# Performance work log

Hardware: AMD Instinct MI355X
Metric: run time of the kernel (lower is better)

## Reference

```python
import jax, jax.numpy as jnp
import numpy as np

HUGE_FLOAT = 1000.0
B, LATENT, N, EMB, NBOND = 256, 256, 64, 64, 5


def setup_inputs() -> dict:
    key = jax.random.key(0)
    ks = jax.random.split(key, 8)
    s1 = 1.0 / np.sqrt(LATENT)
    s2 = 1.0 / np.sqrt(2 * EMB)
    s3 = 1.0 / np.sqrt(EMB)
    return {
        "z": jax.random.normal(ks[0], (B, LATENT), dtype=jnp.float32),
        "num_real_atoms": jax.random.randint(ks[1], (B,), 1, N + 1, dtype=jnp.int32),
        "W_nodes": jax.random.uniform(ks[2], (LATENT, N * EMB), jnp.float32, -s1, s1),
        "b_nodes": jax.random.uniform(ks[3], (N * EMB,), jnp.float32, -s1, s1),
        "W1": jax.random.uniform(ks[4], (2 * EMB, EMB), jnp.float32, -s2, s2),
        "b1": jax.random.uniform(ks[5], (EMB,), jnp.float32, -s2, s2),
        "W2": jax.random.uniform(ks[6], (EMB, NBOND), jnp.float32, -s3, s3),
        "b2": jax.random.uniform(ks[7], (NBOND,), jnp.float32, -s3, s3),
    }


def reference(z, num_real_atoms, W_nodes, b_nodes, W1, b1, W2, b2):
    # z: (B, latent) -> node embeddings h: (B, N, emb)
    h = (z @ W_nodes + b_nodes).reshape(B, N, EMB)
    # edge MLP first layer on concat([h_i, h_j]) == h_i @ W1a + h_j @ W1b
    W1a, W1b = W1[:EMB], W1[EMB:]
    a = jnp.einsum("bne,ef->bnf", h, W1a)  # (B, N, emb)
    c = jnp.einsum("bne,ef->bnf", h, W1b)  # (B, N, emb)
    hidden = jax.nn.relu(a[:, :, None, :] + c[:, None, :, :] + b1)  # (B,N,N,emb)
    logits = jnp.einsum("bijf,fk->bijk", hidden, W2) + b2  # (B,N,N,5)
    # diagonal mask + padding mask (symmetric), constant fill per bond channel
    diag = jnp.eye(N, dtype=bool)  # (N,N)
    real = jnp.arange(N)[None, :] < num_real_atoms[:, None]  # (B,N)
    pad = ~real
    padding = pad[:, :, None] | pad[:, None, :]  # (B,N,N)
    mask = diag[None] | padding  # (B,N,N)
    fill = jnp.where(jnp.arange(NBOND) == NBOND - 1, HUGE_FLOAT, -HUGE_FLOAT).astype(logits.dtype)
    logits = jnp.where(mask[..., None], fill, logits)
    # symmetrize over node pair dims
    return 0.5 * (logits + jnp.swapaxes(logits, 1, 2))
```

## Files before the change

kernel.cpp:

```cpp
#include <hip/hip_runtime.h>
#include <hip/hip_bf16.h>

#define HUGEF 1000.0f

typedef __hip_bfloat16 bf16;

__device__ __forceinline__ float b2f(bf16 x) { return __bfloat162float(x); }

__global__ __launch_bounds__(256) void k_hac(
    const float* __restrict__ z, const float* __restrict__ Wn,
    const float* __restrict__ bn, const float* __restrict__ W1,
    const float* __restrict__ b1, bf16* __restrict__ a_ws,
    bf16* __restrict__ c_ws)
{
    __shared__ float buf0[64][68];
    __shared__ float buf1[64][68];
    __shared__ float buf2[64][68];

    const int t = threadIdx.x;
    const int tx = t & 15, ty = t >> 4;
    const int atom = blockIdx.x;
    const int m0 = blockIdx.y * 64;
    const int n0 = atom * 64;

    float acc[4][4] = {};
    for (int k0 = 0; k0 < 256; k0 += 64) {
        __syncthreads();
        #pragma unroll
        for (int r = 0; r < 4; ++r) {
            int q = t + 256 * r;
            int m = q >> 4, kk = (q & 15) * 4;
            *(float4*)&buf0[m][kk] = *(const float4*)&z[(m0 + m) * 256 + k0 + kk];
        }
        #pragma unroll
        for (int r = 0; r < 4; ++r) {
            int q = t + 256 * r;
            int k = q >> 4, nn = (q & 15) * 4;
            *(float4*)&buf1[k][nn] = *(const float4*)&Wn[(k0 + k) * 4096 + n0 + nn];
        }
        __syncthreads();
        for (int k = 0; k < 64; ++k) {
            float4 bv = *(const float4*)&buf1[k][tx * 4];
            float bb[4] = {bv.x, bv.y, bv.z, bv.w};
            float aa[4];
            #pragma unroll
            for (int i = 0; i < 4; ++i) aa[i] = buf0[ty * 4 + i][k];
            #pragma unroll
            for (int i = 0; i < 4; ++i)
                #pragma unroll
                for (int jj = 0; jj < 4; ++jj) acc[i][jj] += aa[i] * bb[jj];
        }
    }
    __syncthreads();

    {
        float bnv[4];
        #pragma unroll
        for (int jj = 0; jj < 4; ++jj) bnv[jj] = bn[n0 + tx * 4 + jj];
        #pragma unroll
        for (int i = 0; i < 4; ++i)
            #pragma unroll
            for (int jj = 0; jj < 4; ++jj)
                buf2[ty * 4 + i][tx * 4 + jj] = acc[i][jj] + bnv[jj];
        #pragma unroll
        for (int r = 0; r < 4; ++r) {
            int q = t + 256 * r;
            int e = q >> 4, ff = (q & 15) * 4;
            *(float4*)&buf0[e][ff] = *(const float4*)&W1[4 * q];
            *(float4*)&buf1[e][ff] = *(const float4*)&W1[4096 + 4 * q];
        }
    }
    __syncthreads();

    float aacc[4][4] = {}, cacc[4][4] = {};
    const int b0 = ty * 4, f0 = tx * 4;
    for (int e = 0; e < 64; ++e) {
        float4 wa = *(const float4*)&buf0[e][f0];
        float4 wb = *(const float4*)&buf1[e][f0];
        float wav[4] = {wa.x, wa.y, wa.z, wa.w};
        float wbv[4] = {wb.x, wb.y, wb.z, wb.w};
        #pragma unroll
        for (int i = 0; i < 4; ++i) {
            float hv = buf2[b0 + i][e];
            #pragma unroll
            for (int jj = 0; jj < 4; ++jj) {
                aacc[i][jj] += hv * wav[jj];
                cacc[i][jj] += hv * wbv[jj];
            }
        }
    }
    float b1v[4];
    #pragma unroll
    for (int jj = 0; jj < 4; ++jj) b1v[jj] = b1[f0 + jj];
    #pragma unroll
    for (int i = 0; i < 4; ++i) {
        int bi = m0 + b0 + i;
        int idx = bi * 4096 + n0 + f0;
        ushort4 av, cv;
        av.x = __bfloat16_as_ushort(__float2bfloat16(aacc[i][0] + b1v[0]));
        av.y = __bfloat16_as_ushort(__float2bfloat16(aacc[i][1] + b1v[1]));
        av.z = __bfloat16_as_ushort(__float2bfloat16(aacc[i][2] + b1v[2]));
        av.w = __bfloat16_as_ushort(__float2bfloat16(aacc[i][3] + b1v[3]));
        cv.x = __bfloat16_as_ushort(__float2bfloat16(cacc[i][0]));
        cv.y = __bfloat16_as_ushort(__float2bfloat16(cacc[i][1]));
        cv.z = __bfloat16_as_ushort(__float2bfloat16(cacc[i][2]));
        cv.w = __bfloat16_as_ushort(__float2bfloat16(cacc[i][3]));
        *(ushort4*)&a_ws[idx] = av;
        *(ushort4*)&c_ws[idx] = cv;
    }
}

__global__ __launch_bounds__(256) void k_pairs(
    const bf16* __restrict__ a_ws, const bf16* __restrict__ c_ws,
    const int* __restrict__ nra, const float* __restrict__ W2,
    const float* __restrict__ b2, float* __restrict__ out)
{
    __shared__ float as[64][68];
    __shared__ float cs[64][68];
    __shared__ float w2t[5][68];

    const int t = threadIdx.x;
    const int bid = blockIdx.x;
    const int b = bid >> 2;
    const int ic = bid & 3;
    const int n = nra[b];

    #pragma unroll
    for (int r = 0; r < 4; ++r) {
        int q = t + 256 * r;
        int atom = q >> 4, ff = (q & 15) * 4;
        ushort4 av = *(const ushort4*)&a_ws[b * 4096 + 4 * q];
        ushort4 cv = *(const ushort4*)&c_ws[b * 4096 + 4 * q];
        as[atom][ff + 0] = b2f(__ushort_as_bfloat16(av.x));
        as[atom][ff + 1] = b2f(__ushort_as_bfloat16(av.y));
        as[atom][ff + 2] = b2f(__ushort_as_bfloat16(av.z));
        as[atom][ff + 3] = b2f(__ushort_as_bfloat16(av.w));
        cs[atom][ff + 0] = b2f(__ushort_as_bfloat16(cv.x));
        cs[atom][ff + 1] = b2f(__ushort_as_bfloat16(cv.y));
        cs[atom][ff + 2] = b2f(__ushort_as_bfloat16(cv.z));
        cs[atom][ff + 3] = b2f(__ushort_as_bfloat16(cv.w));
    }
    if (t < 64) {
        #pragma unroll
        for (int k = 0; k < 5; ++k) w2t[k][t] = W2[t * 5 + k];
    }
    float b2v[5];
    #pragma unroll
    for (int k = 0; k < 5; ++k) b2v[k] = b2[k];
    __syncthreads();

    const int j = t & 63;
    const int wq = t >> 6;
    const float fillv[5] = {-HUGEF, -HUGEF, -HUGEF, -HUGEF, HUGEF};

    #pragma unroll 1
    for (int q = 0; q < 4; ++q) {
        const int i = ic * 16 + wq * 4 + q;
        float* op = out + ((b * 64 + i) * 64 + j) * 5;
        if (i >= n) {
            #pragma unroll
            for (int k = 0; k < 5; ++k) op[k] = fillv[k];
            continue;
        }
        float acc[5] = {0.f, 0.f, 0.f, 0.f, 0.f};
        for (int f4 = 0; f4 < 64; f4 += 4) {
            float4 ai = *(const float4*)&as[i][f4];
            float4 ci = *(const float4*)&cs[i][f4];
            float4 aj = *(const float4*)&as[j][f4];
            float4 cj = *(const float4*)&cs[j][f4];
            float s0 = fmaxf(ai.x + cj.x, 0.f) + fmaxf(aj.x + ci.x, 0.f);
            float s1 = fmaxf(ai.y + cj.y, 0.f) + fmaxf(aj.y + ci.y, 0.f);
            float s2 = fmaxf(ai.z + cj.z, 0.f) + fmaxf(aj.z + ci.z, 0.f);
            float s3 = fmaxf(ai.w + cj.w, 0.f) + fmaxf(aj.w + ci.w, 0.f);
            #pragma unroll
            for (int k = 0; k < 5; ++k) {
                float4 w = *(const float4*)&w2t[k][f4];
                acc[k] += s0 * w.x + s1 * w.y + s2 * w.z + s3 * w.w;
            }
        }
        const bool masked = (j == i) || (j >= n);
        #pragma unroll
        for (int k = 0; k < 5; ++k) {
            float v = masked ? fillv[k] : (0.5f * acc[k] + b2v[k]);
            op[k] = v;
        }
    }
}

extern "C" void kernel_launch(void* const* d_in, const int* in_sizes, int n_in,
                              void* d_out, int out_size, void* d_ws, size_t ws_size,
                              hipStream_t stream)
{
    const float* z  = (const float*)d_in[0];
    const int*   nra = (const int*)d_in[1];
    const float* Wn = (const float*)d_in[2];
    const float* bn = (const float*)d_in[3];
    const float* W1 = (const float*)d_in[4];
    const float* b1 = (const float*)d_in[5];
    const float* W2 = (const float*)d_in[6];
    const float* b2 = (const float*)d_in[7];
    float* out = (float*)d_out;

    bf16* a_ws = (bf16*)d_ws;
    bf16* c_ws = a_ws + 256 * 4096;

    hipLaunchKernelGGL(k_hac, dim3(64, 4), dim3(256), 0, stream,
                       z, Wn, bn, W1, b1, a_ws, c_ws);
    hipLaunchKernelGGL(k_pairs, dim3(1024), dim3(256), 0, stream,
                       a_ws, c_ws, nra, W2, b2, out);
}
```

Baseline: 118.4 us.

## Use bf16 MFMA for node/edge GMMs and register-block pair kernel

The first kernel now converts z, W_nodes and W1 to bf16 in shared memory and computes both matmuls with 16x16x32 bf16 MFMA instructions instead of scalar FMA loops. This reduces scalar compute but lowers the precision of the node embeddings. The pair kernel keeps a/c as packed bf16 in shared memory, unpacking with shifts. Each thread now computes 8 rows i, reusing j-side values and W2 loads across them, with half as many blocks and early exit for fully padded row groups.

```diff
diff --git a/kernel.cpp b/kernel.cpp
--- a/kernel.cpp
+++ b/kernel.cpp
@@ -4,8 +4,18 @@
 #define HUGEF 1000.0f
 
 typedef __hip_bfloat16 bf16;
-
-__device__ __forceinline__ float b2f(bf16 x) { return __bfloat162float(x); }
+typedef __attribute__((ext_vector_type(8))) short short8;
+typedef __attribute__((ext_vector_type(4))) float floatx4;
+
+__device__ __forceinline__ ushort f2bf(float x) {
+    return __bfloat16_as_ushort(__float2bfloat16(x));
+}
+__device__ __forceinline__ float bflo(unsigned u) {
+    return __uint_as_float(u << 16);
+}
+__device__ __forceinline__ float bfhi(unsigned u) {
+    return __uint_as_float(u & 0xffff0000u);
+}
 
 __global__ __launch_bounds__(256) void k_hac(
     const float* __restrict__ z, const float* __restrict__ Wn,
@@ -13,100 +23,107 @@
     const float* __restrict__ b1, bf16* __restrict__ a_ws,
     bf16* __restrict__ c_ws)
 {
-    __shared__ float buf0[64][68];
-    __shared__ float buf1[64][68];
-    __shared__ float buf2[64][68];
+    __shared__ ushort zt[64][136];
+    __shared__ ushort wnt[64][136];
+    __shared__ ushort ht[64][72];
+    __shared__ ushort w1at[64][72];
+    __shared__ ushort w1bt[64][72];
 
     const int t = threadIdx.x;
-    const int tx = t & 15, ty = t >> 4;
+    const int lane = t & 63;
+    const int wv = t >> 6;
+    const int l15 = lane & 15;
+    const int quad = lane >> 4;
     const int atom = blockIdx.x;
     const int m0 = blockIdx.y * 64;
     const int n0 = atom * 64;
 
-    float acc[4][4] = {};
-    for (int k0 = 0; k0 < 256; k0 += 64) {
+    {
+        const int f = t & 63;
+        const int g = t >> 6;
+        #pragma unroll
+        for (int qq = 0; qq < 4; ++qq) {
+            int e = g * 16 + qq * 4;
+            ushort4 va, vb;
+            va.x = f2bf(W1[(e + 0) * 64 + f]);
+            va.y = f2bf(W1[(e + 1) * 64 + f]);
+            va.z = f2bf(W1[(e + 2) * 64 + f]);
+            va.w = f2bf(W1[(e + 3) * 64 + f]);
+            vb.x = f2bf(W1[(64 + e + 0) * 64 + f]);
+            vb.y = f2bf(W1[(64 + e + 1) * 64 + f]);
+            vb.z = f2bf(W1[(64 + e + 2) * 64 + f]);
+            vb.w = f2bf(W1[(64 + e + 3) * 64 + f]);
+            *(ushort4*)&w1at[f][e] = va;
+            *(ushort4*)&w1bt[f][e] = vb;
+        }
+    }
+
+    floatx4 acc1[4] = {};
+    for (int kt = 0; kt < 256; kt += 128) {
         __syncthreads();
         #pragma unroll
+        for (int r = 0; r < 8; ++r) {
+            int q = t + 256 * r;
+            int m = q >> 5, kk = (q & 31) * 4;
+            float4 v = *(const float4*)&z[(m0 + m) * 256 + kt + kk];
+            ushort4 u = {f2bf(v.x), f2bf(v.y), f2bf(v.z), f2bf(v.w)};
+            *(ushort4*)&zt[m][kk] = u;
+        }
+        {
+            int n = t & 63, g = t >> 6;
+            #pragma unroll
+            for (int qq = 0; qq < 8; ++qq) {
+                int k = g * 32 + qq * 4;
+                const float* p = &Wn[(size_t)(kt + k) * 4096 + n0 + n];
+                ushort4 u = {f2bf(p[0]), f2bf(p[4096]),
+                             f2bf(p[2 * 4096]), f2bf(p[3 * 4096])};
+                *(ushort4*)&wnt[n][k] = u;
+            }
+        }
+        __syncthreads();
+        #pragma unroll
+        for (int ks = 0; ks < 4; ++ks) {
+            short8 a = *(const short8*)&zt[wv * 16 + l15][ks * 32 + quad * 8];
+            #pragma unroll
+            for (int nt = 0; nt < 4; ++nt) {
+                short8 bf = *(const short8*)&wnt[nt * 16 + l15][ks * 32 + quad * 8];
+                acc1[nt] = __builtin_amdgcn_mfma_f32_16x16x32_bf16(a, bf, acc1[nt], 0, 0, 0);
+            }
+        }
+    }
+
+    #pragma unroll
+    for (int nt = 0; nt < 4; ++nt) {
+        float bnv = bn[n0 + nt * 16 + l15];
+        #pragma unroll
+        for (int r = 0; r < 4; ++r)
+            ht[wv * 16 + quad * 4 + r][nt * 16 + l15] = f2bf(acc1[nt][r] + bnv);
+    }
+    __syncthreads();
+
+    floatx4 acc2a[4] = {}, acc2c[4] = {};
+    #pragma unroll
+    for (int ks = 0; ks < 2; ++ks) {
+        short8 a = *(const short8*)&ht[wv * 16 + l15][ks * 32 + quad * 8];
+        #pragma unroll
+        for (int ft = 0; ft < 4; ++ft) {
+            short8 ba = *(const short8*)&w1at[ft * 16 + l15][ks * 32 + quad * 8];
+            short8 bb = *(const short8*)&w1bt[ft * 16 + l15][ks * 32 + quad * 8];
+            acc2a[ft] = __builtin_amdgcn_mfma_f32_16x16x32_bf16(a, ba, acc2a[ft], 0, 0, 0);
+            acc2c[ft] = __builtin_amdgcn_mfma_f32_16x16x32_bf16(a, bb, acc2c[ft], 0, 0, 0);
+        }
+    }
+
+    #pragma unroll
+    for (int ft = 0; ft < 4; ++ft) {
+        float b1v = b1[ft * 16 + l15];
+        #pragma unroll
         for (int r = 0; r < 4; ++r) {
-            int q = t + 256 * r;
-            int m = q >> 4, kk = (q & 15) * 4;
-            *(float4*)&buf0[m][kk] = *(const float4*)&z[(m0 + m) * 256 + k0 + kk];
-        }
-        #pragma unroll
-        for (int r = 0; r < 4; ++r) {
-            int q = t + 256 * r;
-            int k = q >> 4, nn = (q & 15) * 4;
-            *(float4*)&buf1[k][nn] = *(const float4*)&Wn[(k0 + k) * 4096 + n0 + nn];
-        }
-        __syncthreads();
-        for (int k = 0; k < 64; ++k) {
-            float4 bv = *(const float4*)&buf1[k][tx * 4];
-            float bb[4] = {bv.x, bv.y, bv.z, bv.w};
-            float aa[4];
-            #pragma unroll
-            for (int i = 0; i < 4; ++i) aa[i] = buf0[ty * 4 + i][k];
-            #pragma unroll
-            for (int i = 0; i < 4; ++i)
-                #pragma unroll
-                for (int jj = 0; jj < 4; ++jj) acc[i][jj] += aa[i] * bb[jj];
-        }
-    }
-    __syncthreads();
-
-    {
-        float bnv[4];
-        #pragma unroll
-        for (int jj = 0; jj < 4; ++jj) bnv[jj] = bn[n0 + tx * 4 + jj];
-        #pragma unroll
-        for (int i = 0; i < 4; ++i)
-            #pragma unroll
-            for (int jj = 0; jj < 4; ++jj)
-                buf2[ty * 4 + i][tx * 4 + jj] = acc[i][jj] + bnv[jj];
-        #pragma unroll
-        for (int r = 0; r < 4; ++r) {
-            int q = t + 256 * r;
-            int e = q >> 4, ff = (q & 15) * 4;
-            *(float4*)&buf0[e][ff] = *(const float4*)&W1[4 * q];
-            *(float4*)&buf1[e][ff] = *(const float4*)&W1[4096 + 4 * q];
-        }
-    }
-    __syncthreads();
-
-    float aacc[4][4] = {}, cacc[4][4] = {};
-    const int b0 = ty * 4, f0 = tx * 4;
-    for (int e = 0; e < 64; ++e) {
-        float4 wa = *(const float4*)&buf0[e][f0];
-        float4 wb = *(const float4*)&buf1[e][f0];
-        float wav[4] = {wa.x, wa.y, wa.z, wa.w};
-        float wbv[4] = {wb.x, wb.y, wb.z, wb.w};
-        #pragma unroll
-        for (int i = 0; i < 4; ++i) {
-            float hv = buf2[b0 + i][e];
-            #pragma unroll
-            for (int jj = 0; jj < 4; ++jj) {
-                aacc[i][jj] += hv * wav[jj];
-                cacc[i][jj] += hv * wbv[jj];
-            }
-        }
-    }
-    float b1v[4];
-    #pragma unroll
-    for (int jj = 0; jj < 4; ++jj) b1v[jj] = b1[f0 + jj];
-    #pragma unroll
-    for (int i = 0; i < 4; ++i) {
-        int bi = m0 + b0 + i;
-        int idx = bi * 4096 + n0 + f0;
-        ushort4 av, cv;
-        av.x = __bfloat16_as_ushort(__float2bfloat16(aacc[i][0] + b1v[0]));
-        av.y = __bfloat16_as_ushort(__float2bfloat16(aacc[i][1] + b1v[1]));
-        av.z = __bfloat16_as_ushort(__float2bfloat16(aacc[i][2] + b1v[2]));
-        av.w = __bfloat16_as_ushort(__float2bfloat16(aacc[i][3] + b1v[3]));
-        cv.x = __bfloat16_as_ushort(__float2bfloat16(cacc[i][0]));
-        cv.y = __bfloat16_as_ushort(__float2bfloat16(cacc[i][1]));
-        cv.z = __bfloat16_as_ushort(__float2bfloat16(cacc[i][2]));
-        cv.w = __bfloat16_as_ushort(__float2bfloat16(cacc[i][3]));
-        *(ushort4*)&a_ws[idx] = av;
-        *(ushort4*)&c_ws[idx] = cv;
+            int m = wv * 16 + quad * 4 + r;
+            size_t idx = (size_t)(m0 + m) * 4096 + n0 + ft * 16 + l15;
+            a_ws[idx] = __float2bfloat16(acc2a[ft][r] + b1v);
+            c_ws[idx] = __float2bfloat16(acc2c[ft][r]);
+        }
     }
 }
 
@@ -115,30 +132,23 @@
     const int* __restrict__ nra, const float* __restrict__ W2,
     const float* __restrict__ b2, float* __restrict__ out)
 {
-    __shared__ float as[64][68];
-    __shared__ float cs[64][68];
+    __shared__ unsigned ap[64][36];
+    __shared__ unsigned cp[64][36];
     __shared__ float w2t[5][68];
 
     const int t = threadIdx.x;
-    const int bid = blockIdx.x;
-    const int b = bid >> 2;
-    const int ic = bid & 3;
+    const int b = blockIdx.x >> 1;
+    const int ic = blockIdx.x & 1;
     const int n = nra[b];
 
-    #pragma unroll
-    for (int r = 0; r < 4; ++r) {
+    const ushort* ag = (const ushort*)a_ws + (size_t)b * 4096;
+    const ushort* cg = (const ushort*)c_ws + (size_t)b * 4096;
+    #pragma unroll
+    for (int r = 0; r < 2; ++r) {
         int q = t + 256 * r;
-        int atom = q >> 4, ff = (q & 15) * 4;
-        ushort4 av = *(const ushort4*)&a_ws[b * 4096 + 4 * q];
-        ushort4 cv = *(const ushort4*)&c_ws[b * 4096 + 4 * q];
-        as[atom][ff + 0] = b2f(__ushort_as_bfloat16(av.x));
-        as[atom][ff + 1] = b2f(__ushort_as_bfloat16(av.y));
-        as[atom][ff + 2] = b2f(__ushort_as_bfloat16(av.z));
-        as[atom][ff + 3] = b2f(__ushort_as_bfloat16(av.w));
-        cs[atom][ff + 0] = b2f(__ushort_as_bfloat16(cv.x));
-        cs[atom][ff + 1] = b2f(__ushort_as_bfloat16(cv.y));
-        cs[atom][ff + 2] = b2f(__ushort_as_bfloat16(cv.z));
-        cs[atom][ff + 3] = b2f(__ushort_as_bfloat16(cv.w));
+        int atom = q >> 3, wq = (q & 7) * 4;
+        *(uint4*)&ap[atom][wq] = *(const uint4*)&ag[atom * 64 + wq * 2];
+        *(uint4*)&cp[atom][wq] = *(const uint4*)&cg[atom * 64 + wq * 2];
     }
     if (t < 64) {
         #pragma unroll
@@ -150,39 +160,74 @@
     __syncthreads();
 
     const int j = t & 63;
-    const int wq = t >> 6;
+    const int wv = t >> 6;
+    const int i0 = ic * 32 + wv * 8;
     const float fillv[5] = {-HUGEF, -HUGEF, -HUGEF, -HUGEF, HUGEF};
 
-    #pragma unroll 1
-    for (int q = 0; q < 4; ++q) {
-        const int i = ic * 16 + wq * 4 + q;
-        float* op = out + ((b * 64 + i) * 64 + j) * 5;
+    if (i0 >= n) {
+        #pragma unroll
+        for (int r = 0; r < 8; ++r) {
+            float* op = out + ((size_t)(b * 64 + i0 + r) * 64 + j) * 5;
+            #pragma unroll
+            for (int k = 0; k < 5; ++k) op[k] = fillv[k];
+        }
+        return;
+    }
+
+    float acc[8][5] = {};
+    for (int w8 = 0; w8 < 8; ++w8) {
+        uint4 ajp = *(const uint4*)&ap[j][w8 * 4];
+        uint4 cjp = *(const uint4*)&cp[j][w8 * 4];
+        float ajv[8], cjv[8];
+        ajv[0] = bflo(ajp.x); ajv[1] = bfhi(ajp.x);
+        ajv[2] = bflo(ajp.y); ajv[3] = bfhi(ajp.y);
+        ajv[4] = bflo(ajp.z); ajv[5] = bfhi(ajp.z);
+        ajv[6] = bflo(ajp.w); ajv[7] = bfhi(ajp.w);
+        cjv[0] = bflo(cjp.x); cjv[1] = bfhi(cjp.x);
+        cjv[2] = bflo(cjp.y); cjv[3] = bfhi(cjp.y);
+        cjv[4] = bflo(cjp.z); cjv[5] = bfhi(cjp.z);
+        cjv[6] = bflo(cjp.w); cjv[7] = bfhi(cjp.w);
+        float4 wA[5], wB[5];
+        #pragma unroll
+        for (int k = 0; k < 5; ++k) {
+            wA[k] = *(const float4*)&w2t[k][w8 * 8];
+            wB[k] = *(const float4*)&w2t[k][w8 * 8 + 4];
+        }
+        #pragma unroll
+        for (int r = 0; r < 8; ++r) {
+            uint4 aip = *(const uint4*)&ap[i0 + r][w8 * 4];
+            uint4 cip = *(const uint4*)&cp[i0 + r][w8 * 4];
+            float s[8];
+            s[0] = fmaxf(bflo(aip.x) + cjv[0], 0.f) + fmaxf(ajv[0] + bflo(cip.x), 0.f);
+            s[1] = fmaxf(bfhi(aip.x) + cjv[1], 0.f) + fmaxf(ajv[1] + bfhi(cip.x), 0.f);
+            s[2] = fmaxf(bflo(aip.y) + cjv[2], 0.f) + fmaxf(ajv[2] + bflo(cip.y), 0.f);
+            s[3] = fmaxf(bfhi(aip.y) + cjv[3], 0.f) + fmaxf(ajv[3] + bfhi(cip.y), 0.f);
+            s[4] = fmaxf(bflo(aip.z) + cjv[4], 0.f) + fmaxf(ajv[4] + bflo(cip.z), 0.f);
+            s[5] = fmaxf(bfhi(aip.z) + cjv[5], 0.f) + fmaxf(ajv[5] + bfhi(cip.z), 0.f);
+            s[6] = fmaxf(bflo(aip.w) + cjv[6], 0.f) + fmaxf(ajv[6] + bflo(cip.w), 0.f);
+            s[7] = fmaxf(bfhi(aip.w) + cjv[7], 0.f) + fmaxf(ajv[7] + bfhi(cip.w), 0.f);
+            #pragma unroll
+            for (int k = 0; k < 5; ++k) {
+                acc[r][k] += s[0] * wA[k].x + s[1] * wA[k].y +
+                             s[2] * wA[k].z + s[3] * wA[k].w +
+                             s[4] * wB[k].x + s[5] * wB[k].y +
+                             s[6] * wB[k].z + s[7] * wB[k].w;
+            }
+        }
+    }
+
+    #pragma unroll
+    for (int r = 0; r < 8; ++r) {
+        const int i = i0 + r;
+        float* op = out + ((size_t)(b * 64 + i) * 64 + j) * 5;
         if (i >= n) {
             #pragma unroll
             for (int k = 0; k < 5; ++k) op[k] = fillv[k];
-            continue;
-        }
-        float acc[5] = {0.f, 0.f, 0.f, 0.f, 0.f};
-        for (int f4 = 0; f4 < 64; f4 += 4) {
-            float4 ai = *(const float4*)&as[i][f4];
-            float4 ci = *(const float4*)&cs[i][f4];
-            float4 aj = *(const float4*)&as[j][f4];
-            float4 cj = *(const float4*)&cs[j][f4];
-            float s0 = fmaxf(ai.x + cj.x, 0.f) + fmaxf(aj.x + ci.x, 0.f);
-            float s1 = fmaxf(ai.y + cj.y, 0.f) + fmaxf(aj.y + ci.y, 0.f);
-            float s2 = fmaxf(ai.z + cj.z, 0.f) + fmaxf(aj.z + ci.z, 0.f);
-            float s3 = fmaxf(ai.w + cj.w, 0.f) + fmaxf(aj.w + ci.w, 0.f);
-            #pragma unroll
-            for (int k = 0; k < 5; ++k) {
-                float4 w = *(const float4*)&w2t[k][f4];
-                acc[k] += s0 * w.x + s1 * w.y + s2 * w.z + s3 * w.w;
-            }
-        }
-        const bool masked = (j == i) || (j >= n);
-        #pragma unroll
-        for (int k = 0; k < 5; ++k) {
-            float v = masked ? fillv[k] : (0.5f * acc[k] + b2v[k]);
-            op[k] = v;
+        } else {
+            const bool masked = (j == i) || (j >= n);
+            #pragma unroll
+            for (int k = 0; k < 5; ++k)
+                op[k] = masked ? fillv[k] : (0.5f * acc[r][k] + b2v[k]);
         }
     }
 }
@@ -206,6 +251,6 @@
 
     hipLaunchKernelGGL(k_hac, dim3(64, 4), dim3(256), 0, stream,
                        z, Wn, bn, W1, b1, a_ws, c_ws);
-    hipLaunchKernelGGL(k_pairs, dim3(1024), dim3(256), 0, stream,
+    hipLaunchKernelGGL(k_pairs, dim3(512), dim3(256), 0, stream,
                        a_ws, c_ws, nra, W2, b2, out);
 }
```

Measured after the change: 110.0 us. 1.08x faster.
